# Optimization experiments

Measured on AMD Instinct MI355X. Metric: run time of the kernel, lower is better.

## Reference

```python
import jax, jax.numpy as jnp
import numpy as np

NUM_HEADS = 8
NUM_GROUPS = 32
EPS = 1e-5
RESCALE = 1.0


def setup_inputs() -> dict:
    key = jax.random.key(0)
    ks = jax.random.split(key, 7)
    b, c, h, w = 16, 512, 32, 32
    return {
        "x": jax.random.normal(ks[0], (b, c, h, w), jnp.float32),
        "norm_w": jax.random.normal(ks[1], (c,), jnp.float32),
        "norm_b": jax.random.normal(ks[2], (c,), jnp.float32),
        "qkv_w": jax.random.normal(ks[3], (3 * c, c), jnp.float32) * (c ** -0.5),
        "qkv_b": jax.random.normal(ks[4], (3 * c,), jnp.float32) * 0.02,
        "proj_w": jax.random.normal(ks[5], (c, c), jnp.float32) * (c ** -0.5),
        "proj_b": jax.random.normal(ks[6], (c,), jnp.float32) * 0.02,
    }


def _group_norm(x, w, b):
    # x: [B, C, L]
    B, C, L = x.shape
    g = x.reshape(B, NUM_GROUPS, (C // NUM_GROUPS) * L)
    mu = jnp.mean(g, axis=-1, keepdims=True)
    var = jnp.var(g, axis=-1, keepdims=True)
    g = (g - mu) * jax.lax.rsqrt(var + EPS)
    return g.reshape(B, C, L) * w[None, :, None] + b[None, :, None]


def reference(x, norm_w, norm_b, qkv_w, qkv_b, proj_w, proj_b):
    b, c, hh, ww = x.shape
    L = hh * ww
    H = NUM_HEADS
    ch = c // H  # head dim

    xr = x.reshape(b, c, L)
    hid = _group_norm(xr, norm_w, norm_b)

    # 1x1 conv1d == matmul over channel dim: [3c, c] @ [b, c, L]
    qkv = jnp.einsum('oc,bcl->bol', qkv_w, hid) + qkv_b[None, :, None]
    # torch: reshape(b*H, 3*ch, L).split(ch) -> per-head contiguous [q|k|v] blocks
    qkv = qkv.reshape(b, H, 3, ch, L)
    q, k, v = qkv[:, :, 0], qkv[:, :, 1], qkv[:, :, 2]  # [b, H, ch, L]

    scale = 1.0 / (ch ** 0.25)
    weight = jnp.einsum('bhct,bhcs->bhts', q * scale, k * scale)
    weight = jax.nn.softmax(weight.astype(jnp.float32), axis=-1).astype(weight.dtype)
    a = jnp.einsum('bhts,bhcs->bhct', weight, v)  # [b, H, ch, L]

    h = a.reshape(b, c, L)
    h = jnp.einsum('oc,bcl->bol', proj_w, h) + proj_b[None, :, None]
    h = h.reshape(b, c, hh, ww)
    return (x + h) / RESCALE
```

## Files before the change

### kernel.cpp

```cpp
#include <hip/hip_runtime.h>
#include <hip/hip_bf16.h>
#include <stdint.h>


using f32x4  = __attribute__((ext_vector_type(4))) float;
using bf16x8 = __attribute__((ext_vector_type(8))) __bf16;
using s8v    = __attribute__((ext_vector_type(8))) short;
using s4v    = __attribute__((ext_vector_type(4))) short;

__device__ __forceinline__ short f2bf(float f){
  union { float f; unsigned u; } c; c.f = f;
  unsigned r = (c.u + 0x7FFFu + ((c.u >> 16) & 1u)) >> 16;
  return (short)r;
}

__device__ __forceinline__ float exp2_fast(float x){
#if __has_builtin(__builtin_amdgcn_exp2f)
  return __builtin_amdgcn_exp2f(x);
#else
  return exp2f(x);
#endif
}

__device__ __forceinline__ void gl_lds16(const void* g, void* l){
  __builtin_amdgcn_global_load_lds((const __attribute__((address_space(1))) void*)g,
                                   (__attribute__((address_space(3))) void*)l, 16, 0, 0);
}

__global__ void k_convw(const float* __restrict__ qw, const float* __restrict__ pw,
                        const float* __restrict__ qb,
                        short* __restrict__ qwb, short* __restrict__ pwb,
                        float* __restrict__ qbp){
  int i = blockIdx.x * 256 + threadIdx.x;
  if (i < 786432){
    int o = i >> 9, kk = i & 511;
    int h = o / 192, rem = o - h*192;
    int nr = (rem >> 6)*512 + h*64 + (rem & 63);
    qwb[nr*512 + kk] = f2bf(qw[i]);
  } else if (i < 1048576){
    int j = i - 786432;
    pwb[j] = f2bf(pw[j]);
  } else if (i < 1050112){
    int o = i - 1048576;
    int h = o / 192, rem = o - h*192;
    qbp[(rem >> 6)*512 + h*64 + (rem & 63)] = qb[o];
  }
}

__global__ __launch_bounds__(256) void k_gnorm(const float* __restrict__ x,
                                               const float* __restrict__ w,
                                               const float* __restrict__ bia,
                                               short* __restrict__ hid){
  int b = blockIdx.x >> 5;
  int g = blockIdx.x & 31;
  int tid = threadIdx.x;
  const float* xg = x + ((size_t)b*512 + g*16)*1024;
  int l0 = tid * 4;
  float v[16][4];
  float s1 = 0.f, s2 = 0.f;
  #pragma unroll
  for (int c = 0; c < 16; c++){
    f32x4 t = *(const f32x4*)(xg + c*1024 + l0);
    #pragma unroll
    for (int j = 0; j < 4; j++){ v[c][j] = t[j]; s1 += t[j]; s2 += t[j]*t[j]; }
  }
  #pragma unroll
  for (int m = 32; m; m >>= 1){ s1 += __shfl_xor(s1, m); s2 += __shfl_xor(s2, m); }
  __shared__ float r1[4], r2[4];
  int wv = tid >> 6, ln = tid & 63;
  if (ln == 0){ r1[wv] = s1; r2[wv] = s2; }
  __syncthreads();
  s1 = r1[0]+r1[1]+r1[2]+r1[3];
  s2 = r2[0]+r2[1]+r2[2]+r2[3];
  float mu = s1 * (1.f/16384.f);
  float var = s2 * (1.f/16384.f) - mu*mu;
  float rs = rsqrtf(var + 1e-5f);
  float ww[16], bb[16];
  #pragma unroll
  for (int c = 0; c < 16; c++){ ww[c] = w[g*16+c]*rs; bb[c] = bia[g*16+c]; }
  #pragma unroll
  for (int j = 0; j < 4; j++){
    short o[16];
    #pragma unroll
    for (int c = 0; c < 16; c++) o[c] = f2bf((v[c][j]-mu)*ww[c] + bb[c]);
    short* dst = hid + ((size_t)(b*1024 + l0 + j))*512 + g*16;
    *(s8v*)dst     = *(s8v*)o;
    *(s8v*)(dst+8) = *(s8v*)(o+8);
  }
}

template<int EPI>
__global__ __launch_bounds__(256) void k_gemm(
    const short* __restrict__ A, const short* __restrict__ Bm,
    const float* __restrict__ bias, const float* __restrict__ xres,
    short* __restrict__ q_t, short* __restrict__ k_t, short* __restrict__ v_t,
    float* __restrict__ outp)
{
  __shared__ short Al[2][128*64];
  __shared__ short Bl[2][128*64];
  int id = blockIdx.x;
  int xcd = id & 7, ix = id >> 3;
  int mt, nt;
  if (EPI == 0){ mt = ix % 12; nt = ix / 12; }
  else         { mt = ix & 3;  nt = ix >> 2; }
  int m0 = mt * 128;
  int n0 = (xcd + 8*nt) * 128;
  int tid = threadIdx.x;
  int lane = tid & 63;
  int wv = tid >> 6;
  int wr = wv >> 1, wc = wv & 1;
  int l15 = lane & 15, g = lane >> 4;
  f32x4 acc[4][4] = {};

  auto STAGE = [&](int db, int k0){
    #pragma unroll
    for (int i = 0; i < 8; i++){
      int cc = wv*8 + i;
      if (cc < 16){
        int slot = cc*64 + lane;
        int row = slot >> 3, off = slot & 7;
        gl_lds16(A + (size_t)(m0+row)*512 + k0 + (off ^ (row&7))*8,
                 (char*)Al[db] + cc*1024);
      } else {
        int slot = (cc-16)*64 + lane;
        int row = slot >> 3, off = slot & 7;
        gl_lds16(Bm + (size_t)(n0+row)*512 + k0 + (off ^ (row&7))*8,
                 (char*)Bl[db] + (cc-16)*1024);
      }
    }
  };

  STAGE(0, 0);
  for (int t = 0; t < 8; t++){
    asm volatile("s_waitcnt vmcnt(0)" ::: "memory");
    __builtin_amdgcn_s_barrier();
    if (t < 7) STAGE((t+1)&1, (t+1)*64);
    int db = t & 1;
    #pragma unroll
    for (int kk = 0; kk < 2; kk++){
      bf16x8 af[4], bf[4];
      #pragma unroll
      for (int m = 0; m < 4; m++){
        int row = wr*64 + m*16 + l15;
        int byte = row*128 + (((kk*64) + (g*16)) ^ ((row&7)<<4));
        af[m] = *(const bf16x8*)((char*)Al[db] + byte);
      }
      #pragma unroll
      for (int n = 0; n < 4; n++){
        int row = wc*64 + n*16 + l15;
        int byte = row*128 + (((kk*64) + (g*16)) ^ ((row&7)<<4));
        bf[n] = *(const bf16x8*)((char*)Bl[db] + byte);
      }
      __builtin_amdgcn_s_setprio(1);
      #pragma unroll
      for (int m = 0; m < 4; m++)
        #pragma unroll
        for (int n = 0; n < 4; n++)
          acc[m][n] = __builtin_amdgcn_mfma_f32_16x16x32_bf16(af[m], bf[n], acc[m][n], 0, 0, 0);
      __builtin_amdgcn_s_setprio(0);
    }
  }
  __builtin_amdgcn_s_barrier();

  if (EPI == 0){
    int sel = m0 >> 9;
    if (sel < 2){
      const float sc = (sel == 0) ? 0.18033688011112042f : 1.0f;
      short* dstb = (sel == 0) ? q_t : k_t;
      #pragma unroll
      for (int m = 0; m < 4; m++){
        int ob = m0 + wr*64 + m*16 + (g<<2);
        int hh = (ob>>6)&7, c0 = ob&63;
        float bs[4];
        #pragma unroll
        for (int r = 0; r < 4; r++) bs[r] = bias[ob+r];
        #pragma unroll
        for (int n = 0; n < 4; n++){
          int nn = n0 + wc*64 + n*16 + l15;
          int bb = nn >> 10, ll = nn & 1023;
          int bh = bb*8 + hh;
          short o4[4];
          #pragma unroll
          for (int r = 0; r < 4; r++) o4[r] = f2bf((acc[m][n][r] + bs[r]) * sc);
          *(s4v*)(dstb + ((size_t)bh*1024 + ll)*64 + c0) = *(s4v*)o4;
        }
      }
    } else {
      short* Sc = (short*)Al;
      #pragma unroll
      for (int m = 0; m < 4; m++){
        int ob = m0 + wr*64 + m*16 + (g<<2);
        int h2 = (ob>>6)&1, cq = (ob>>4)&3;
        float bs[4];
        #pragma unroll
        for (int r = 0; r < 4; r++) bs[r] = bias[ob+r];
        #pragma unroll
        for (int n = 0; n < 4; n++){
          int nn = n0 + wc*64 + n*16 + l15;
          int sl = nn & 63, sreg = (nn>>6)&1;
          int ks2 = sl >> 5, gq = (sl>>2)&3, i2 = (sl&3) + 4*((sl>>4)&1);
          int base = (h2*2 + sreg)*4096 + (((ks2*4+gq)*4 + cq)*16 + (g<<2))*8 + i2;
          #pragma unroll
          for (int r = 0; r < 4; r++)
            Sc[base + r*8] = f2bf(acc[m][n][r] + bs[r]);
        }
      }
      __syncthreads();
      int b0  = n0 >> 10;
      int s64 = (n0 >> 6) & 15;
      int hb  = (m0 - 1024) >> 6;
      #pragma unroll
      for (int it = 0; it < 8; it++){
        int flat = it*2048 + tid*8;
        int h2 = flat >> 13, rem = flat & 8191, sreg = rem >> 12, off = rem & 4095;
        int bh = b0*8 + hb + h2;
        *(s8v*)(v_t + ((size_t)bh*16 + s64 + sreg)*4096 + off) = *(const s8v*)(Sc + flat);
      }
    }
  } else {
    #pragma unroll
    for (int m = 0; m < 4; m++){
      int ob = m0 + wr*64 + m*16 + (g<<2);
      float bs[4];
      #pragma unroll
      for (int r = 0; r < 4; r++) bs[r] = bias[ob+r];
      #pragma unroll
      for (int n = 0; n < 4; n++){
        int nn = n0 + wc*64 + n*16 + l15;
        int bb = nn >> 10, ll = nn & 1023;
        #pragma unroll
        for (int r = 0; r < 4; r++){
          size_t idx = ((size_t)bb*512 + ob + r)*1024 + ll;
          outp[idx] = xres[idx] + acc[m][n][r] + bs[r];
        }
      }
    }
  }
}

__global__ __launch_bounds__(256, 4) void k_attn(
    const short* __restrict__ q_t, const short* __restrict__ k_t,
    const short* __restrict__ v_t, short* __restrict__ a_bt)
{
  __shared__ short Kl[2][64*64];
  __shared__ short Vl[2][64*64];
  int id = blockIdx.x;
  int xcd = id & 7, ix = id >> 3;
  int bh = xcd*16 + (ix >> 3);
  int qb = ix & 7;
  int bb = bh >> 3, hh = bh & 7;
  int tid = threadIdx.x;
  int lane = tid & 63;
  int wv = tid >> 6;
  int l15 = lane & 15, g = lane >> 4;

  bf16x8 qf[2][2];
  #pragma unroll
  for (int qt = 0; qt < 2; qt++){
    const short* qbase = q_t + ((size_t)bh*1024 + qb*128 + qt*64 + wv*16 + l15)*64 + g*8;
    qf[qt][0] = *(const bf16x8*)(qbase);
    qf[qt][1] = *(const bf16x8*)(qbase + 32);
  }
  asm volatile("" :: "v"(qf[0][0]), "v"(qf[0][1]), "v"(qf[1][0]), "v"(qf[1][1]));

  bf16x8 onesb;
  #pragma unroll
  for (int i = 0; i < 8; i++) onesb[i] = (__bf16)1.0f;

  auto STAGE = [&](int db, int s0){
    #pragma unroll
    for (int i = 0; i < 4; i++){
      int cc = wv*4 + i;
      if (cc < 8){
        int slot = cc*64 + lane;
        int row = slot >> 3, off = slot & 7;
        gl_lds16(k_t + ((size_t)bh*1024 + s0 + row)*64 + (off ^ (row&7))*8,
                 (char*)Kl[db] + cc*1024);
      } else {
        gl_lds16(v_t + ((size_t)bh*16 + (s0>>6))*4096 + (cc-8)*512 + lane*8,
                 (char*)Vl[db] + (cc-8)*1024);
      }
    }
  };

  f32x4 o[2][4] = {};
  f32x4 osum[2] = {};

  STAGE(0, 0);
  for (int t = 0; t < 16; t++){
    asm volatile("s_waitcnt vmcnt(0)" ::: "memory");
    __builtin_amdgcn_s_barrier();
    if (t < 15) STAGE((t+1)&1, (t+1)*64);
    int db = t & 1;

    f32x4 sc[2][4] = {};
    #pragma unroll
    for (int j = 0; j < 4; j++){
      bf16x8 kf0, kf1;
      {
        int row = j*16 + l15;
        int swz = (row&7)<<4;
        kf0 = *(const bf16x8*)((char*)Kl[db] + row*128 + ((g*16) ^ swz));
        kf1 = *(const bf16x8*)((char*)Kl[db] + row*128 + ((64 + g*16) ^ swz));
      }
      __builtin_amdgcn_s_setprio(1);
      #pragma unroll
      for (int qt = 0; qt < 2; qt++){
        sc[qt][j] = __builtin_amdgcn_mfma_f32_16x16x32_bf16(kf0, qf[qt][0], sc[qt][j], 0, 0, 0);
        sc[qt][j] = __builtin_amdgcn_mfma_f32_16x16x32_bf16(kf1, qf[qt][1], sc[qt][j], 0, 0, 0);
      }
      __builtin_amdgcn_s_setprio(0);
    }

    #pragma unroll
    for (int ks = 0; ks < 2; ks++){
      bf16x8 pa[2];
      #pragma unroll
      for (int qt = 0; qt < 2; qt++){
        #pragma unroll
        for (int i2 = 0; i2 < 8; i2++)
          pa[qt][i2] = (__bf16)exp2_fast(sc[qt][2*ks + (i2>>2)][i2&3]);
        osum[qt] = __builtin_amdgcn_mfma_f32_16x16x32_bf16(pa[qt], onesb, osum[qt], 0, 0, 0);
      }
      #pragma unroll
      for (int jd = 0; jd < 4; jd++){
        bf16x8 vbb = *(const bf16x8*)((char*)Vl[db] + ((ks*4+g)*4+jd)*256 + l15*16);
        __builtin_amdgcn_s_setprio(1);
        #pragma unroll
        for (int qt = 0; qt < 2; qt++)
          o[qt][jd] = __builtin_amdgcn_mfma_f32_16x16x32_bf16(pa[qt], vbb, o[qt][jd], 0, 0, 0);
        __builtin_amdgcn_s_setprio(0);
      }
    }
  }

  #pragma unroll
  for (int qt = 0; qt < 2; qt++){
    #pragma unroll
    for (int r = 0; r < 4; r++){
      float inv = 1.f / osum[qt][r];
      int qrow = qb*128 + qt*64 + wv*16 + g*4 + r;
      #pragma unroll
      for (int jd = 0; jd < 4; jd++)
        a_bt[((size_t)bb*1024 + qrow)*512 + hh*64 + jd*16 + l15] = f2bf(o[qt][jd][r] * inv);
    }
  }
}

extern "C" void kernel_launch(void* const* d_in, const int* in_sizes, int n_in,
                              void* d_out, int out_size, void* d_ws, size_t ws_size,
                              hipStream_t stream){
  const float* x  = (const float*)d_in[0];
  const float* nw = (const float*)d_in[1];
  const float* nb = (const float*)d_in[2];
  const float* qw = (const float*)d_in[3];
  const float* qb = (const float*)d_in[4];
  const float* pw = (const float*)d_in[5];
  const float* pb = (const float*)d_in[6];
  float* outp = (float*)d_out;

  char* ws = (char*)d_ws;
  short* hid  = (short*)(ws);
  short* qwb  = (short*)(ws + 16777216);
  short* pwb  = (short*)(ws + 18350080);
  short* q_t  = (short*)(ws + 18874368);
  short* k_t  = (short*)(ws + 35651584);
  short* v_t  = (short*)(ws + 52428800);
  short* a_bt = hid;
  float* qbp  = (float*)d_out;
  if (ws_size < 69206016) return;

  k_convw<<<4103, 256, 0, stream>>>(qw, pw, qb, qwb, pwb, qbp);
  k_gnorm<<<512, 256, 0, stream>>>(x, nw, nb, hid);
  k_gemm<0><<<1536, 256, 0, stream>>>(qwb, hid, qbp, nullptr, q_t, k_t, v_t, nullptr);
  k_attn<<<1024, 256, 0, stream>>>(q_t, k_t, v_t, a_bt);
  k_gemm<1><<<512, 256, 0, stream>>>(pwb, a_bt, pb, x, nullptr, nullptr, nullptr, outp);
}
```

Baseline: 123.4 us.

## Use 4-stage LDS ring with smaller K slices in GEMM and attention

```diff
diff --git a/kernel.cpp b/kernel.cpp
--- a/kernel.cpp
+++ b/kernel.cpp
@@ -96,8 +96,8 @@
     short* __restrict__ q_t, short* __restrict__ k_t, short* __restrict__ v_t,
     float* __restrict__ outp)
 {
-  __shared__ short Al[2][128*64];
-  __shared__ short Bl[2][128*64];
+  __shared__ short Al[4*4096];
+  __shared__ short Bl[4*4096];
   int id = blockIdx.x;
   int xcd = id & 7, ix = id >> 3;
   int mt, nt;
@@ -112,54 +112,59 @@
   int l15 = lane & 15, g = lane >> 4;
   f32x4 acc[4][4] = {};
 
-  auto STAGE = [&](int db, int k0){
-    #pragma unroll
-    for (int i = 0; i < 8; i++){
-      int cc = wv*8 + i;
-      if (cc < 16){
-        int slot = cc*64 + lane;
-        int row = slot >> 3, off = slot & 7;
-        gl_lds16(A + (size_t)(m0+row)*512 + k0 + (off ^ (row&7))*8,
-                 (char*)Al[db] + cc*1024);
-      } else {
-        int slot = (cc-16)*64 + lane;
-        int row = slot >> 3, off = slot & 7;
-        gl_lds16(Bm + (size_t)(n0+row)*512 + k0 + (off ^ (row&7))*8,
-                 (char*)Bl[db] + (cc-16)*1024);
-      }
+  auto STAGE = [&](int db, int t){
+    int k0 = t * 32;
+    #pragma unroll
+    for (int i = 0; i < 4; i++){
+      int cc = wv*4 + i;
+      int c2 = cc & 7;
+      int row = c2*16 + (lane>>2), slot = lane & 3;
+      const short* src = (cc < 8 ? A + (size_t)(m0+row)*512
+                                 : Bm + (size_t)(n0+row)*512)
+                         + k0 + ((slot ^ ((row>>1)&3))*8);
+      char* dst = (char*)(cc < 8 ? Al : Bl) + db*8192 + c2*1024;
+      gl_lds16(src, dst);
     }
   };
 
+  auto COMPUTE = [&](int db){
+    const char* Ab = (const char*)Al + db*8192;
+    const char* Bb = (const char*)Bl + db*8192;
+    bf16x8 af[4], bf[4];
+    #pragma unroll
+    for (int m = 0; m < 4; m++){
+      int row = wr*64 + m*16 + l15;
+      af[m] = *(const bf16x8*)(Ab + row*64 + ((g*16) ^ (((row>>1)&3)<<4)));
+    }
+    #pragma unroll
+    for (int n = 0; n < 4; n++){
+      int row = wc*64 + n*16 + l15;
+      bf[n] = *(const bf16x8*)(Bb + row*64 + ((g*16) ^ (((row>>1)&3)<<4)));
+    }
+    __builtin_amdgcn_s_setprio(1);
+    #pragma unroll
+    for (int m = 0; m < 4; m++)
+      #pragma unroll
+      for (int n = 0; n < 4; n++)
+        acc[m][n] = __builtin_amdgcn_mfma_f32_16x16x32_bf16(af[m], bf[n], acc[m][n], 0, 0, 0);
+    __builtin_amdgcn_s_setprio(0);
+  };
+
   STAGE(0, 0);
-  for (int t = 0; t < 8; t++){
-    asm volatile("s_waitcnt vmcnt(0)" ::: "memory");
+  STAGE(1, 1);
+  #pragma unroll 2
+  for (int t = 0; t < 14; t++){
+    STAGE((t+2)&3, t+2);
+    asm volatile("s_waitcnt vmcnt(8)" ::: "memory");
     __builtin_amdgcn_s_barrier();
-    if (t < 7) STAGE((t+1)&1, (t+1)*64);
-    int db = t & 1;
-    #pragma unroll
-    for (int kk = 0; kk < 2; kk++){
-      bf16x8 af[4], bf[4];
-      #pragma unroll
-      for (int m = 0; m < 4; m++){
-        int row = wr*64 + m*16 + l15;
-        int byte = row*128 + (((kk*64) + (g*16)) ^ ((row&7)<<4));
-        af[m] = *(const bf16x8*)((char*)Al[db] + byte);
-      }
-      #pragma unroll
-      for (int n = 0; n < 4; n++){
-        int row = wc*64 + n*16 + l15;
-        int byte = row*128 + (((kk*64) + (g*16)) ^ ((row&7)<<4));
-        bf[n] = *(const bf16x8*)((char*)Bl[db] + byte);
-      }
-      __builtin_amdgcn_s_setprio(1);
-      #pragma unroll
-      for (int m = 0; m < 4; m++)
-        #pragma unroll
-        for (int n = 0; n < 4; n++)
-          acc[m][n] = __builtin_amdgcn_mfma_f32_16x16x32_bf16(af[m], bf[n], acc[m][n], 0, 0, 0);
-      __builtin_amdgcn_s_setprio(0);
-    }
-  }
+    COMPUTE(t&3);
+  }
+  asm volatile("s_waitcnt vmcnt(4)" ::: "memory");
+  __builtin_amdgcn_s_barrier();
+  COMPUTE(2);
+  asm volatile("s_waitcnt vmcnt(0)" ::: "memory");
+  __builtin_amdgcn_s_barrier();
+  COMPUTE(3);
   __builtin_amdgcn_s_barrier();
 
   if (EPI == 0){
@@ -242,8 +247,8 @@
     const short* __restrict__ q_t, const short* __restrict__ k_t,
     const short* __restrict__ v_t, short* __restrict__ a_bt)
 {
-  __shared__ short Kl[2][64*64];
-  __shared__ short Vl[2][64*64];
+  __shared__ short Kh[4*2048];
+  __shared__ short Vh[4*2048];
   int id = blockIdx.x;
   int xcd = id & 7, ix = id >> 3;
   int bh = xcd*16 + (ix >> 3);
@@ -267,72 +272,77 @@
   #pragma unroll
   for (int i = 0; i < 8; i++) onesb[i] = (__bf16)1.0f;
 
-  auto STAGE = [&](int db, int s0){
-    #pragma unroll
-    for (int i = 0; i < 4; i++){
-      int cc = wv*4 + i;
-      if (cc < 8){
-        int slot = cc*64 + lane;
-        int row = slot >> 3, off = slot & 7;
-        gl_lds16(k_t + ((size_t)bh*1024 + s0 + row)*64 + (off ^ (row&7))*8,
-                 (char*)Kl[db] + cc*1024);
-      } else {
-        gl_lds16(v_t + ((size_t)bh*16 + (s0>>6))*4096 + (cc-8)*512 + lane*8,
-                 (char*)Vl[db] + (cc-8)*1024);
-      }
-    }
-  };
-
   f32x4 o[2][4] = {};
   f32x4 osum[2] = {};
 
+  auto STAGE = [&](int db, int h){
+    int t64 = h >> 1, ks = h & 1;
+    #pragma unroll
+    for (int i = 0; i < 2; i++){
+      int cc = wv*2 + i;
+      if (cc < 4){
+        int row = cc*8 + (lane>>3), slot = lane & 7;
+        gl_lds16(k_t + ((size_t)bh*1024 + h*32 + row)*64 + ((slot ^ (row&7))*8),
+                 (char*)Kh + db*4096 + cc*1024);
+      } else {
+        gl_lds16(v_t + ((size_t)bh*16 + t64)*4096 + ks*2048 + (cc-4)*512 + lane*8,
+                 (char*)Vh + db*4096 + (cc-4)*1024);
+      }
+    }
+  };
+
+  auto COMPUTE = [&](int db){
+    const char* Kb = (const char*)Kh + db*4096;
+    const char* Vb = (const char*)Vh + db*4096;
+    f32x4 scl[2][2] = {};
+    #pragma unroll
+    for (int jl = 0; jl < 2; jl++){
+      int row = jl*16 + l15;
+      int swz = (row&7)<<4;
+      bf16x8 kf0 = *(const bf16x8*)(Kb + row*128 + ((g*16) ^ swz));
+      bf16x8 kf1 = *(const bf16x8*)(Kb + row*128 + ((64 + g*16) ^ swz));
+      __builtin_amdgcn_s_setprio(1);
+      #pragma unroll
+      for (int qt = 0; qt < 2; qt++){
+        scl[qt][jl] = __builtin_amdgcn_mfma_f32_16x16x32_bf16(kf0, qf[qt][0], scl[qt][jl], 0, 0, 0);
+        scl[qt][jl] = __builtin_amdgcn_mfma_f32_16x16x32_bf16(kf1, qf[qt][1], scl[qt][jl], 0, 0, 0);
+      }
+      __builtin_amdgcn_s_setprio(0);
+    }
+    bf16x8 pa[2];
+    #pragma unroll
+    for (int qt = 0; qt < 2; qt++){
+      #pragma unroll
+      for (int i2 = 0; i2 < 8; i2++)
+        pa[qt][i2] = (__bf16)exp2_fast(scl[qt][i2>>2][i2&3]);
+      osum[qt] = __builtin_amdgcn_mfma_f32_16x16x32_bf16(pa[qt], onesb, osum[qt], 0, 0, 0);
+    }
+    #pragma unroll
+    for (int jd = 0; jd < 4; jd++){
+      bf16x8 vbb = *(const bf16x8*)(Vb + (g*4+jd)*256 + l15*16);
+      __builtin_amdgcn_s_setprio(1);
+      #pragma unroll
+      for (int qt = 0; qt < 2; qt++)
+        o[qt][jd] = __builtin_amdgcn_mfma_f32_16x16x32_bf16(pa[qt], vbb, o[qt][jd], 0, 0, 0);
+      __builtin_amdgcn_s_setprio(0);
+    }
+  };
+
   STAGE(0, 0);
-  for (int t = 0; t < 16; t++){
-    asm volatile("s_waitcnt vmcnt(0)" ::: "memory");
+  STAGE(1, 1);
+  #pragma unroll 2
+  for (int h = 0; h < 30; h++){
+    STAGE((h+2)&3, h+2);
+    asm volatile("s_waitcnt vmcnt(4)" ::: "memory");
     __builtin_amdgcn_s_barrier();
-    if (t < 15) STAGE((t+1)&1, (t+1)*64);
-    int db = t & 1;
-
-    f32x4 sc[2][4] = {};
-    #pragma unroll
-    for (int j = 0; j < 4; j++){
-      bf16x8 kf0, kf1;
-      {
-        int row = j*16 + l15;
-        int swz = (row&7)<<4;
-        kf0 = *(const bf16x8*)((char*)Kl[db] + row*128 + ((g*16) ^ swz));
-        kf1 = *(const bf16x8*)((char*)Kl[db] + row*128 + ((64 + g*16) ^ swz));
-      }
-      __builtin_amdgcn_s_setprio(1);
-      #pragma unroll
-      for (int qt = 0; qt < 2; qt++){
-        sc[qt][j] = __builtin_amdgcn_mfma_f32_16x16x32_bf16(kf0, qf[qt][0], sc[qt][j], 0, 0, 0);
-        sc[qt][j] = __builtin_amdgcn_mfma_f32_16x16x32_bf16(kf1, qf[qt][1], sc[qt][j], 0, 0, 0);
-      }
-      __builtin_amdgcn_s_setprio(0);
-    }
-
-    #pragma unroll
-    for (int ks = 0; ks < 2; ks++){
-      bf16x8 pa[2];
-      #pragma unroll
-      for (int qt = 0; qt < 2; qt++){
-        #pragma unroll
-        for (int i2 = 0; i2 < 8; i2++)
-          pa[qt][i2] = (__bf16)exp2_fast(sc[qt][2*ks + (i2>>2)][i2&3]);
-        osum[qt] = __builtin_amdgcn_mfma_f32_16x16x32_bf16(pa[qt], onesb, osum[qt], 0, 0, 0);
-      }
-      #pragma unroll
-      for (int jd = 0; jd < 4; jd++){
-        bf16x8 vbb = *(const bf16x8*)((char*)Vl[db] + ((ks*4+g)*4+jd)*256 + l15*16);
-        __builtin_amdgcn_s_setprio(1);
-        #pragma unroll
-        for (int qt = 0; qt < 2; qt++)
-          o[qt][jd] = __builtin_amdgcn_mfma_f32_16x16x32_bf16(pa[qt], vbb, o[qt][jd], 0, 0, 0);
-        __builtin_amdgcn_s_setprio(0);
-      }
-    }
-  }
+    COMPUTE(h&3);
+  }
+  asm volatile("s_waitcnt vmcnt(2)" ::: "memory");
+  __builtin_amdgcn_s_barrier();
+  COMPUTE(2);
+  asm volatile("s_waitcnt vmcnt(0)" ::: "memory");
+  __builtin_amdgcn_s_barrier();
+  COMPUTE(3);
 
   #pragma unroll
   for (int qt = 0; qt < 2; qt++){
```

Measured after the change: 123.8 us. About the same (+0.4%).
